# Optimization experiments

Hardware: AMD Instinct MI355X
Metric: run time of the kernel (lower is better)

The kernel has to match this reference:

```python
import jax, jax.numpy as jnp
import numpy as np

B, T, H = 16, 512, 512

def _gru_layer(x, h0, wih, whh, bih, bhh, reverse):
    # x: [B,T,in], h0: [B,H]; PyTorch gate order r,z,n in the 3H axis.
    xg = jnp.einsum('bti,gi->btg', x, wih) + bih  # [B,T,3H] input-side gates, precomputed
    def step(h, xg_t):
        gh = h @ whh.T + bhh  # [B,3H]
        xr, xz, xn = jnp.split(xg_t, 3, axis=-1)
        hr, hz, hn = jnp.split(gh, 3, axis=-1)
        r = jax.nn.sigmoid(xr + hr)
        z = jax.nn.sigmoid(xz + hz)
        n = jnp.tanh(xn + r * hn)
        h_new = (1.0 - z) * n + z * h
        return h_new, h_new
    _, ys = jax.lax.scan(step, h0, jnp.swapaxes(xg, 0, 1), reverse=reverse)  # [T,B,H]
    return jnp.swapaxes(ys, 0, 1)

def _forward(x, h1, h2,
             wih_l0f, whh_l0f, bih_l0f, bhh_l0f, wih_l0b, whh_l0b, bih_l0b, bhh_l0b,
             wih_l1f, whh_l1f, bih_l1f, bhh_l1f, wih_l1b, whh_l1b, bih_l1b, bhh_l1b,
             wih_l2f, whh_l2f, bih_l2f, bhh_l2f, wih_l2b, whh_l2b, bih_l2b, bhh_l2b,
             g2_wih, g2_whh, g2_bih, g2_bhh, fc_w, fc_b):
    layers = [((wih_l0f, whh_l0f, bih_l0f, bhh_l0f), (wih_l0b, whh_l0b, bih_l0b, bhh_l0b)),
              ((wih_l1f, whh_l1f, bih_l1f, bhh_l1f), (wih_l1b, whh_l1b, bih_l1b, bhh_l1b)),
              ((wih_l2f, whh_l2f, bih_l2f, bhh_l2f), (wih_l2b, whh_l2b, bih_l2b, bhh_l2b))]
    out = x
    for l, (pf, pb) in enumerate(layers):
        of = _gru_layer(out, h1[2 * l], *pf, reverse=False)
        ob = _gru_layer(out, h1[2 * l + 1], *pb, reverse=True)
        out = jnp.concatenate([of, ob], axis=-1)  # [B,T,2H]
    out2 = _gru_layer(out, h2[0], g2_wih, g2_whh, g2_bih, g2_bhh, reverse=False)  # [B,T,H]
    logits = out2[:, -1, :] @ fc_w.T + fc_b  # [B,1]
    return (jax.nn.sigmoid(logits), out2)

def setup_inputs():
    key = jax.random.key(0)
    ks = jax.random.split(key, 40)
    cnt = iter(range(40))
    s = jnp.float32(0.04)
    d = {}
    d['x'] = jax.random.normal(ks[next(cnt)], (B, T, 2048), jnp.float32)
    d['h1'] = jax.random.normal(ks[next(cnt)], (6, B, H), jnp.float32) * s
    d['h2'] = jax.random.normal(ks[next(cnt)], (1, B, H), jnp.float32) * s
    in_dims = [2048, 2 * H, 2 * H]
    for l in range(3):
        for dr in 'fb':
            d[f'wih_l{l}{dr}'] = jax.random.normal(ks[next(cnt)], (3 * H, in_dims[l]), jnp.float32) * s
            d[f'whh_l{l}{dr}'] = jax.random.normal(ks[next(cnt)], (3 * H, H), jnp.float32) * s
            d[f'bih_l{l}{dr}'] = jax.random.normal(ks[next(cnt)], (3 * H,), jnp.float32) * s
            d[f'bhh_l{l}{dr}'] = jax.random.normal(ks[next(cnt)], (3 * H,), jnp.float32) * s
    d['g2_wih'] = jax.random.normal(ks[next(cnt)], (3 * H, 2 * H), jnp.float32) * s
    d['g2_whh'] = jax.random.normal(ks[next(cnt)], (3 * H, H), jnp.float32) * s
    d['g2_bih'] = jax.random.normal(ks[next(cnt)], (3 * H,), jnp.float32) * s
    d['g2_bhh'] = jax.random.normal(ks[next(cnt)], (3 * H,), jnp.float32) * s
    d['fc_w'] = jax.random.normal(ks[next(cnt)], (1, H), jnp.float32) * s
    d['fc_b'] = jax.random.normal(ks[next(cnt)], (1,), jnp.float32) * s
    return d

def reference(x, h1, h2,
              wih_l0f, whh_l0f, bih_l0f, bhh_l0f, wih_l0b, whh_l0b, bih_l0b, bhh_l0b,
              wih_l1f, whh_l1f, bih_l1f, bhh_l1f, wih_l1b, whh_l1b, bih_l1b, bhh_l1b,
              wih_l2f, whh_l2f, bih_l2f, bhh_l2f, wih_l2b, whh_l2b, bih_l2b, bhh_l2b,
              g2_wih, g2_whh, g2_bih, g2_bhh, fc_w, fc_b):
    return _forward(x, h1, h2,
                    wih_l0f, whh_l0f, bih_l0f, bhh_l0f, wih_l0b, whh_l0b, bih_l0b, bhh_l0b,
                    wih_l1f, whh_l1f, bih_l1f, bhh_l1f, wih_l1b, whh_l1b, bih_l1b, bhh_l1b,
                    wih_l2f, whh_l2f, bih_l2f, bhh_l2f, wih_l2b, whh_l2b, bih_l2b, bhh_l2b,
                    g2_wih, g2_whh, g2_bih, g2_bhh, fc_w, fc_b)
```

## Files before the change

### kernel.cpp

```cpp
#include <hip/hip_runtime.h>
#include <cstdint>
#include <cstddef>

typedef unsigned short u16;
typedef unsigned int u32;
typedef __attribute__((ext_vector_type(8))) short bf16x8;
typedef __attribute__((ext_vector_type(4))) float f32x4;

#define T_SEQ 512
#define HID 512

__device__ __forceinline__ u16 f2bf(float f) {
  union { float f; u32 i; } c; c.f = f;
  u32 r = (c.i + 0x7FFFu + ((c.i >> 16) & 1u)) >> 16;
  return (u16)r;
}
__device__ __forceinline__ u16 f2h(float f) {
  union { _Float16 h; u16 u; } c; c.h = (_Float16)f; return c.u;
}
__device__ __forceinline__ float h2f(u16 u) {
  union { u16 u; _Float16 h; } c; c.u = u; return (float)c.h;
}
__device__ __forceinline__ float sigmf(float x) { return 1.f / (1.f + __expf(-x)); }
__device__ __forceinline__ float tanhfast(float x) {
  float e = __expf(2.f * x); return 1.f - 2.f / (e + 1.f);
}

template <int AF32>
__launch_bounds__(256)
__global__ void gemm_xg(const void* __restrict__ Av,
                        const float* __restrict__ W0, const float* __restrict__ W1,
                        const float* __restrict__ b0, const float* __restrict__ b1,
                        u16* __restrict__ xg0, u16* __restrict__ xg1, int K) {
  const int dir = blockIdx.z;
  const float* W = dir ? W1 : W0;
  const float* bias = dir ? b1 : b0;
  u16* xg = dir ? xg1 : xg0;
  const int bm = blockIdx.x, bn = blockIdx.y;
  const int tid = threadIdx.x, lane = tid & 63, wv = tid >> 6;
  const int wm = wv & 1, wn = wv >> 1, quad = lane >> 4, l15 = lane & 15;

  __shared__ u16 As[128 * 40];
  __shared__ u16 Bs[128 * 40];

  f32x4 acc[4][4] = {};
  const float* Wb = W + (size_t)(bn * 128) * K;

  for (int k0 = 0; k0 < K; k0 += 32) {
    __syncthreads();
    if constexpr (AF32) {
      const float* Ab = (const float*)Av + (size_t)(bm * 128) * K;
#pragma unroll
      for (int it = 0; it < 4; ++it) {
        int c = tid + it * 256;
        int row = c >> 3, kp = (c & 7) * 4;
        float4 v = *(const float4*)(Ab + (size_t)row * K + k0 + kp);
        ushort4 s = { f2bf(v.x), f2bf(v.y), f2bf(v.z), f2bf(v.w) };
        *(ushort4*)(&As[row * 40 + kp]) = s;
      }
    } else {
      const u16* Ab = (const u16*)Av + (size_t)(bm * 128) * K;
#pragma unroll
      for (int it = 0; it < 2; ++it) {
        int c = tid + it * 256;
        int row = c >> 2, kp = (c & 3) * 8;
        *(bf16x8*)(&As[row * 40 + kp]) = *(const bf16x8*)(Ab + (size_t)row * K + k0 + kp);
      }
    }
#pragma unroll
    for (int it = 0; it < 4; ++it) {
      int c = tid + it * 256;
      int row = c >> 3, kp = (c & 7) * 4;
      float4 v = *(const float4*)(Wb + (size_t)row * K + k0 + kp);
      ushort4 s = { f2bf(v.x), f2bf(v.y), f2bf(v.z), f2bf(v.w) };
      *(ushort4*)(&Bs[row * 40 + kp]) = s;
    }
    __syncthreads();
    bf16x8 af[4], bf[4];
#pragma unroll
    for (int i = 0; i < 4; ++i) {
      af[i] = *(const bf16x8*)(&As[(wm * 64 + i * 16 + l15) * 40 + quad * 8]);
      bf[i] = *(const bf16x8*)(&Bs[(wn * 64 + i * 16 + l15) * 40 + quad * 8]);
    }
#pragma unroll
    for (int mi = 0; mi < 4; ++mi)
#pragma unroll
      for (int ni = 0; ni < 4; ++ni)
        acc[mi][ni] = __builtin_amdgcn_mfma_f32_16x16x32_bf16(af[mi], bf[ni], acc[mi][ni], 0, 0, 0);
  }

#pragma unroll
  for (int ni = 0; ni < 4; ++ni) {
    int n = bn * 128 + wn * 64 + ni * 16 + l15;
    float bv = bias[n];
#pragma unroll
    for (int mi = 0; mi < 4; ++mi) {
      int m0 = bm * 128 + wm * 64 + mi * 16 + quad * 4;
#pragma unroll
      for (int r = 0; r < 4; ++r)
        xg[(size_t)(m0 + r) * 1536 + n] = f2h(acc[mi][ni][r] + bv);
    }
  }
}

__launch_bounds__(384, 1)
__global__ void gru_rec(const u16* __restrict__ xg_f, const u16* __restrict__ xg_b,
                        const float* __restrict__ whh_f, const float* __restrict__ whh_b,
                        const float* __restrict__ bhh_f, const float* __restrict__ bhh_b,
                        const float* __restrict__ h0_f, const float* __restrict__ h0_b,
                        void* __restrict__ outp, int out_stride, int out_f32,
                        u16* __restrict__ hbuf, int* __restrict__ counters, int Tn) {
  const int dir = blockIdx.y;
  const u16* xg   = dir ? xg_b  : xg_f;
  const float* whh = dir ? whh_b : whh_f;
  const float* bhh = dir ? bhh_b : bhh_f;
  const float* h0  = dir ? h0_b  : h0_f;
  const int w = blockIdx.x;
  const int tid = threadIdx.x, lane = tid & 63, wv = tid >> 6;
  const int quad = lane >> 4, l15 = lane & 15;
  int* cnt = counters + dir * 1024;
  u16* hb0 = hbuf + (dir * 2 + 0) * (16 * 512);
  u16* hb1 = hbuf + (dir * 2 + 1) * (16 * 512);
  const int dir_off = dir * 512;

  __shared__ float glds[3][16][64];
  __shared__ float hprev[16][64];
  __shared__ u16 xlds[3][16][64];
  __shared__ float bhl[3][64];

  bf16x8 bfr[2][16];
#pragma unroll
  for (int f = 0; f < 2; ++f) {
    int fl = wv * 2 + f;
    int g = fl >> 2, q = fl & 3;
    int row = g * 512 + (w * 4 + q) * 16 + l15;
    const float* wp = whh + (size_t)row * 512 + quad * 8;
#pragma unroll
    for (int kt = 0; kt < 16; ++kt) {
      float4 a = *(const float4*)(wp + kt * 32);
      float4 b = *(const float4*)(wp + kt * 32 + 4);
      bf16x8 fr;
      fr[0] = (short)f2bf(a.x); fr[1] = (short)f2bf(a.y);
      fr[2] = (short)f2bf(a.z); fr[3] = (short)f2bf(a.w);
      fr[4] = (short)f2bf(b.x); fr[5] = (short)f2bf(b.y);
      fr[6] = (short)f2bf(b.z); fr[7] = (short)f2bf(b.w);
      bfr[f][kt] = fr;
    }
  }
  for (int i = tid; i < 512; i += 384) {
    int b = i >> 5, j2 = (i & 31) * 2;
    float v0 = h0[b * 512 + w * 64 + j2];
    float v1 = h0[b * 512 + w * 64 + j2 + 1];
    hprev[b][j2] = v0; hprev[b][j2 + 1] = v1;
    u32 pk = (u32)f2bf(v0) | ((u32)f2bf(v1) << 16);
    __hip_atomic_store((u32*)(hb1 + b * 512 + w * 64 + j2), pk,
                       __ATOMIC_RELAXED, __HIP_MEMORY_SCOPE_AGENT);
  }
  for (int i = tid; i < 192; i += 384) {
    int g = i >> 6, jl = i & 63;
    bhl[g][jl] = bhh[g * 512 + w * 64 + jl];
  }
  __syncthreads();
  if (tid == 0)
    __hip_atomic_fetch_add(&cnt[0], 1, __ATOMIC_RELEASE, __HIP_MEMORY_SCOPE_AGENT);

  for (int t = 0; t < Tn; ++t) {
    const int te = dir ? (Tn - 1 - t) : t;
    for (int i = tid; i < 768; i += 384) {
      int g = i >> 8, r2 = i & 255, b = r2 >> 4, j4 = (r2 & 15) * 4;
      uint2 v = *(const uint2*)(xg + ((size_t)(b * Tn + te)) * 1536 + g * 512 + w * 64 + j4);
      *(uint2*)(&xlds[g][b][j4]) = v;
    }
    if (tid == 0) {
      while (__hip_atomic_load(&cnt[t], __ATOMIC_RELAXED, __HIP_MEMORY_SCOPE_AGENT) < 8)
        __builtin_amdgcn_s_sleep(1);
      (void)__hip_atomic_load(&cnt[t], __ATOMIC_ACQUIRE, __HIP_MEMORY_SCOPE_AGENT);
    }
    __syncthreads();

    const u16* hsrc = (t & 1) ? hb0 : hb1;
    const u16* hp = hsrc + l15 * 512 + quad * 8;
    bf16x8 afr[16];
#pragma unroll
    for (int kt = 0; kt < 16; ++kt) afr[kt] = *(const bf16x8*)(hp + kt * 32);

#pragma unroll
    for (int f = 0; f < 2; ++f) {
      f32x4 acc = {0.f, 0.f, 0.f, 0.f};
#pragma unroll
      for (int kt = 0; kt < 16; ++kt)
        acc = __builtin_amdgcn_mfma_f32_16x16x32_bf16(afr[kt], bfr[f][kt], acc, 0, 0, 0);
      int fl = wv * 2 + f, g = fl >> 2, q = fl & 3;
#pragma unroll
      for (int r = 0; r < 4; ++r) glds[g][quad * 4 + r][q * 16 + l15] = acc[r];
    }
    __syncthreads();

    u16* hbw = (t & 1) ? hb1 : hb0;
    for (int i = tid; i < 512; i += 384) {
      int b = i >> 5, j2 = (i & 31) * 2;
      float hn2[2];
#pragma unroll
      for (int u = 0; u < 2; ++u) {
        int jl = j2 + u;
        float xr = h2f(xlds[0][b][jl]);
        float xz = h2f(xlds[1][b][jl]);
        float xn = h2f(xlds[2][b][jl]);
        float hr = glds[0][b][jl] + bhl[0][jl];
        float hz = glds[1][b][jl] + bhl[1][jl];
        float hnn = glds[2][b][jl] + bhl[2][jl];
        float r = sigmf(xr + hr);
        float z = sigmf(xz + hz);
        float n = tanhfast(xn + r * hnn);
        float hv = (1.f - z) * n + z * hprev[b][jl];
        hprev[b][jl] = hv;
        hn2[u] = hv;
      }
      u32 pk = (u32)f2bf(hn2[0]) | ((u32)f2bf(hn2[1]) << 16);
      __hip_atomic_store((u32*)(hbw + b * 512 + w * 64 + j2), pk,
                         __ATOMIC_RELAXED, __HIP_MEMORY_SCOPE_AGENT);
      if (out_f32) {
        float2 o = { hn2[0], hn2[1] };
        *(float2*)((float*)outp + (size_t)(b * Tn + te) * out_stride + dir_off + w * 64 + j2) = o;
      } else {
        *(u32*)((u16*)outp + (size_t)(b * Tn + te) * out_stride + dir_off + w * 64 + j2) = pk;
      }
    }
    __syncthreads();
    if (tid == 0)
      __hip_atomic_fetch_add(&cnt[t + 1], 1, __ATOMIC_RELEASE, __HIP_MEMORY_SCOPE_AGENT);
  }
}

__global__ void fc_kernel(const float* __restrict__ out2, const float* __restrict__ fc_w,
                          const float* __restrict__ fc_b, float* __restrict__ dst) {
  int b = blockIdx.x, lane = threadIdx.x;
  const float* row = out2 + ((size_t)b * T_SEQ + (T_SEQ - 1)) * HID;
  float s = 0.f;
  for (int j = lane; j < HID; j += 64) s += row[j] * fc_w[j];
#pragma unroll
  for (int off = 32; off > 0; off >>= 1) s += __shfl_down(s, off, 64);
  if (lane == 0) dst[b] = sigmf(s + fc_b[0]);
}

extern "C" void kernel_launch(void* const* d_in, const int* in_sizes, int n_in,
                              void* d_out, int out_size, void* d_ws, size_t ws_size,
                              hipStream_t stream) {
  const float* x  = (const float*)d_in[0];
  const float* h1 = (const float*)d_in[1];
  const float* h2 = (const float*)d_in[2];
  auto P = [&](int i) { return (const float*)d_in[i]; };

  u16* xg0 = (u16*)d_ws;
  u16* xg1 = xg0 + (size_t)8192 * 1536;
  u16* outb = xg1 + (size_t)8192 * 1536;
  u16* hbuf = outb + (size_t)8192 * 1024;
  int* counters = (int*)(hbuf + 4 * 8192);
  float* out_f = (float*)d_out;
  float* out2 = out_f + 16;

  hipMemsetAsync(counters, 0, 8192 * sizeof(int), stream);

  gemm_xg<1><<<dim3(64, 12, 2), 256, 0, stream>>>(x, P(3), P(7), P(5), P(9), xg0, xg1, 2048);
  gru_rec<<<dim3(8, 2), 384, 0, stream>>>(xg0, xg1, P(4), P(8), P(6), P(10),
                                          h1, h1 + 8192, outb, 1024, 0, hbuf, counters, T_SEQ);
  gemm_xg<0><<<dim3(64, 12, 2), 256, 0, stream>>>(outb, P(11), P(15), P(13), P(17), xg0, xg1, 1024);
  gru_rec<<<dim3(8, 2), 384, 0, stream>>>(xg0, xg1, P(12), P(16), P(14), P(18),
                                          h1 + 2 * 8192, h1 + 3 * 8192, outb, 1024, 0, hbuf,
                                          counters + 2048, T_SEQ);
  gemm_xg<0><<<dim3(64, 12, 2), 256, 0, stream>>>(outb, P(19), P(23), P(21), P(25), xg0, xg1, 1024);
  gru_rec<<<dim3(8, 2), 384, 0, stream>>>(xg0, xg1, P(20), P(24), P(22), P(26),
                                          h1 + 4 * 8192, h1 + 5 * 8192, outb, 1024, 0, hbuf,
                                          counters + 4096, T_SEQ);
  gemm_xg<0><<<dim3(64, 12, 1), 256, 0, stream>>>(outb, P(27), P(27), P(29), P(29), xg0, xg1, 1024);
  gru_rec<<<dim3(8, 1), 384, 0, stream>>>(xg0, xg0, P(28), P(28), P(30), P(30),
                                          h2, h2, out2, 512, 1, hbuf, counters + 6144, T_SEQ);
  fc_kernel<<<16, 64, 0, stream>>>(out2, P(31), P(32), out_f);
}
```

Before: 11.89 ms.

## Restructure GRU recurrence so each wave owns all three gates with per-wave flags

Rewrites the recurrent kernel so that each wave computes the r, z and n gate columns for its own 16 hidden units. r and z weights stay in registers and the n weights sit in LDS, so the gate nonlinearity runs directly on the MFMA accumulators with no LDS round trip and no block-wide barriers. The grid drops to 4 blocks of 512 threads per direction. Cross-block synchronisation moves from one shared counter per timestep to a flag per wave, polled by a single wave-wide load. The change also prefetches xg straight into registers, and in exchange adds 32-way flag polling and uses 128KB of LDS per block.

```diff
diff --git a/kernel.cpp b/kernel.cpp
--- a/kernel.cpp
+++ b/kernel.cpp
@@ -24,6 +24,16 @@
 __device__ __forceinline__ float sigmf(float x) { return 1.f / (1.f + __expf(-x)); }
 __device__ __forceinline__ float tanhfast(float x) {
   float e = __expf(2.f * x); return 1.f - 2.f / (e + 1.f);
+}
+__device__ __forceinline__ bf16x8 pack8(const float* p) {
+  float4 a = *(const float4*)(p);
+  float4 b = *(const float4*)(p + 4);
+  bf16x8 fr;
+  fr[0] = (short)f2bf(a.x); fr[1] = (short)f2bf(a.y);
+  fr[2] = (short)f2bf(a.z); fr[3] = (short)f2bf(a.w);
+  fr[4] = (short)f2bf(b.x); fr[5] = (short)f2bf(b.y);
+  fr[6] = (short)f2bf(b.z); fr[7] = (short)f2bf(b.w);
+  return fr;
 }
 
 template <int AF32>
@@ -76,17 +86,17 @@
       *(ushort4*)(&Bs[row * 40 + kp]) = s;
     }
     __syncthreads();
-    bf16x8 af[4], bf[4];
+    bf16x8 af[4], bfv[4];
 #pragma unroll
     for (int i = 0; i < 4; ++i) {
       af[i] = *(const bf16x8*)(&As[(wm * 64 + i * 16 + l15) * 40 + quad * 8]);
-      bf[i] = *(const bf16x8*)(&Bs[(wn * 64 + i * 16 + l15) * 40 + quad * 8]);
+      bfv[i] = *(const bf16x8*)(&Bs[(wn * 64 + i * 16 + l15) * 40 + quad * 8]);
     }
 #pragma unroll
     for (int mi = 0; mi < 4; ++mi)
 #pragma unroll
       for (int ni = 0; ni < 4; ++ni)
-        acc[mi][ni] = __builtin_amdgcn_mfma_f32_16x16x32_bf16(af[mi], bf[ni], acc[mi][ni], 0, 0, 0);
+        acc[mi][ni] = __builtin_amdgcn_mfma_f32_16x16x32_bf16(af[mi], bfv[ni], acc[mi][ni], 0, 0, 0);
   }
 
 #pragma unroll
@@ -103,7 +113,7 @@
   }
 }
 
-__launch_bounds__(384, 1)
+__launch_bounds__(512, 2)
 __global__ void gru_rec(const u16* __restrict__ xg_f, const u16* __restrict__ xg_b,
                         const float* __restrict__ whh_f, const float* __restrict__ whh_b,
                         const float* __restrict__ bhh_f, const float* __restrict__ bhh_b,
@@ -118,117 +128,123 @@
   const int w = blockIdx.x;
   const int tid = threadIdx.x, lane = tid & 63, wv = tid >> 6;
   const int quad = lane >> 4, l15 = lane & 15;
-  int* cnt = counters + dir * 1024;
+  const int gcol = w * 128 + wv * 16 + l15;
+  int* flg = counters + dir * 1024;
   u16* hb0 = hbuf + (dir * 2 + 0) * (16 * 512);
   u16* hb1 = hbuf + (dir * 2 + 1) * (16 * 512);
   const int dir_off = dir * 512;
 
-  __shared__ float glds[3][16][64];
-  __shared__ float hprev[16][64];
-  __shared__ u16 xlds[3][16][64];
-  __shared__ float bhl[3][64];
+  __shared__ u16 nlds[8 * 8192];
 
   bf16x8 bfr[2][16];
-#pragma unroll
-  for (int f = 0; f < 2; ++f) {
-    int fl = wv * 2 + f;
-    int g = fl >> 2, q = fl & 3;
-    int row = g * 512 + (w * 4 + q) * 16 + l15;
-    const float* wp = whh + (size_t)row * 512 + quad * 8;
+  {
+    const float* wr = whh + (size_t)(0 * 512 + gcol) * 512 + quad * 8;
+    const float* wz = whh + (size_t)(1 * 512 + gcol) * 512 + quad * 8;
+    const float* wn = whh + (size_t)(2 * 512 + gcol) * 512 + quad * 8;
 #pragma unroll
     for (int kt = 0; kt < 16; ++kt) {
-      float4 a = *(const float4*)(wp + kt * 32);
-      float4 b = *(const float4*)(wp + kt * 32 + 4);
-      bf16x8 fr;
-      fr[0] = (short)f2bf(a.x); fr[1] = (short)f2bf(a.y);
-      fr[2] = (short)f2bf(a.z); fr[3] = (short)f2bf(a.w);
-      fr[4] = (short)f2bf(b.x); fr[5] = (short)f2bf(b.y);
-      fr[6] = (short)f2bf(b.z); fr[7] = (short)f2bf(b.w);
-      bfr[f][kt] = fr;
-    }
-  }
-  for (int i = tid; i < 512; i += 384) {
-    int b = i >> 5, j2 = (i & 31) * 2;
-    float v0 = h0[b * 512 + w * 64 + j2];
-    float v1 = h0[b * 512 + w * 64 + j2 + 1];
-    hprev[b][j2] = v0; hprev[b][j2 + 1] = v1;
-    u32 pk = (u32)f2bf(v0) | ((u32)f2bf(v1) << 16);
-    __hip_atomic_store((u32*)(hb1 + b * 512 + w * 64 + j2), pk,
-                       __ATOMIC_RELAXED, __HIP_MEMORY_SCOPE_AGENT);
-  }
-  for (int i = tid; i < 192; i += 384) {
-    int g = i >> 6, jl = i & 63;
-    bhl[g][jl] = bhh[g * 512 + w * 64 + jl];
-  }
-  __syncthreads();
-  if (tid == 0)
-    __hip_atomic_fetch_add(&cnt[0], 1, __ATOMIC_RELEASE, __HIP_MEMORY_SCOPE_AGENT);
+      bfr[0][kt] = pack8(wr + kt * 32);
+      bfr[1][kt] = pack8(wz + kt * 32);
+      *(bf16x8*)(&nlds[wv * 8192 + kt * 512 + lane * 8]) = pack8(wn + kt * 32);
+    }
+  }
+  const float bh0 = bhh[0 * 512 + gcol];
+  const float bh1 = bhh[1 * 512 + gcol];
+  const float bh2 = bhh[2 * 512 + gcol];
+
+  float hv[4];
+#pragma unroll
+  for (int r = 0; r < 4; ++r) hv[r] = h0[(quad * 4 + r) * 512 + gcol];
+#pragma unroll
+  for (int r = 0; r < 4; ++r) {
+    u32 hb = (u32)f2bf(hv[r]);
+    u32 pb = (u32)__shfl_xor((int)hb, 1, 64);
+    if (!(lane & 1))
+      __hip_atomic_store((u32*)(hb1 + (quad * 4 + r) * 512 + gcol), hb | (pb << 16),
+                         __ATOMIC_RELAXED, __HIP_MEMORY_SCOPE_AGENT);
+  }
+  if (lane == 0)
+    __hip_atomic_store(&flg[w * 8 + wv], 1, __ATOMIC_RELEASE, __HIP_MEMORY_SCOPE_AGENT);
 
   for (int t = 0; t < Tn; ++t) {
     const int te = dir ? (Tn - 1 - t) : t;
-    for (int i = tid; i < 768; i += 384) {
-      int g = i >> 8, r2 = i & 255, b = r2 >> 4, j4 = (r2 & 15) * 4;
-      uint2 v = *(const uint2*)(xg + ((size_t)(b * Tn + te)) * 1536 + g * 512 + w * 64 + j4);
-      *(uint2*)(&xlds[g][b][j4]) = v;
-    }
-    if (tid == 0) {
-      while (__hip_atomic_load(&cnt[t], __ATOMIC_RELAXED, __HIP_MEMORY_SCOPE_AGENT) < 8)
+
+    u16 xv[12];
+    {
+      const u16* xb = xg + (size_t)te * 1536 + gcol;
+#pragma unroll
+      for (int r = 0; r < 4; ++r)
+#pragma unroll
+        for (int g = 0; g < 3; ++g)
+          xv[r * 3 + g] = xb[(size_t)(quad * 4 + r) * Tn * 1536 + g * 512];
+    }
+
+    {
+      const int target = t + 1;
+      while (1) {
+        int v = (lane < 32)
+            ? __hip_atomic_load(&flg[lane], __ATOMIC_RELAXED, __HIP_MEMORY_SCOPE_AGENT)
+            : 0x7fffffff;
+        if (__all(v >= target)) break;
         __builtin_amdgcn_s_sleep(1);
-      (void)__hip_atomic_load(&cnt[t], __ATOMIC_ACQUIRE, __HIP_MEMORY_SCOPE_AGENT);
-    }
-    __syncthreads();
-
-    const u16* hsrc = (t & 1) ? hb0 : hb1;
-    const u16* hp = hsrc + l15 * 512 + quad * 8;
+      }
+      __builtin_amdgcn_fence(__ATOMIC_ACQUIRE, "agent");
+    }
+
+    const u16* hp = ((t & 1) ? hb0 : hb1) + l15 * 512 + quad * 8;
     bf16x8 afr[16];
 #pragma unroll
     for (int kt = 0; kt < 16; ++kt) afr[kt] = *(const bf16x8*)(hp + kt * 32);
 
-#pragma unroll
-    for (int f = 0; f < 2; ++f) {
-      f32x4 acc = {0.f, 0.f, 0.f, 0.f};
-#pragma unroll
-      for (int kt = 0; kt < 16; ++kt)
-        acc = __builtin_amdgcn_mfma_f32_16x16x32_bf16(afr[kt], bfr[f][kt], acc, 0, 0, 0);
-      int fl = wv * 2 + f, g = fl >> 2, q = fl & 3;
-#pragma unroll
-      for (int r = 0; r < 4; ++r) glds[g][quad * 4 + r][q * 16 + l15] = acc[r];
-    }
-    __syncthreads();
+    f32x4 accr = {0.f, 0.f, 0.f, 0.f}, accz = accr, accn = accr;
+#pragma unroll
+    for (int kt = 0; kt < 16; ++kt) {
+      bf16x8 nf = *(const bf16x8*)(&nlds[wv * 8192 + kt * 512 + lane * 8]);
+      accr = __builtin_amdgcn_mfma_f32_16x16x32_bf16(afr[kt], bfr[0][kt], accr, 0, 0, 0);
+      accz = __builtin_amdgcn_mfma_f32_16x16x32_bf16(afr[kt], bfr[1][kt], accz, 0, 0, 0);
+      accn = __builtin_amdgcn_mfma_f32_16x16x32_bf16(afr[kt], nf, accn, 0, 0, 0);
+    }
+
+#pragma unroll
+    for (int r = 0; r < 4; ++r) {
+      float xr = h2f(xv[r * 3 + 0]);
+      float xz = h2f(xv[r * 3 + 1]);
+      float xn = h2f(xv[r * 3 + 2]);
+      float rg = sigmf(xr + accr[r] + bh0);
+      float zg = sigmf(xz + accz[r] + bh1);
+      float ng = tanhfast(xn + rg * (accn[r] + bh2));
+      hv[r] = (1.f - zg) * ng + zg * hv[r];
+    }
 
     u16* hbw = (t & 1) ? hb1 : hb0;
-    for (int i = tid; i < 512; i += 384) {
-      int b = i >> 5, j2 = (i & 31) * 2;
-      float hn2[2];
-#pragma unroll
-      for (int u = 0; u < 2; ++u) {
-        int jl = j2 + u;
-        float xr = h2f(xlds[0][b][jl]);
-        float xz = h2f(xlds[1][b][jl]);
-        float xn = h2f(xlds[2][b][jl]);
-        float hr = glds[0][b][jl] + bhl[0][jl];
-        float hz = glds[1][b][jl] + bhl[1][jl];
-        float hnn = glds[2][b][jl] + bhl[2][jl];
-        float r = sigmf(xr + hr);
-        float z = sigmf(xz + hz);
-        float n = tanhfast(xn + r * hnn);
-        float hv = (1.f - z) * n + z * hprev[b][jl];
-        hprev[b][jl] = hv;
-        hn2[u] = hv;
-      }
-      u32 pk = (u32)f2bf(hn2[0]) | ((u32)f2bf(hn2[1]) << 16);
-      __hip_atomic_store((u32*)(hbw + b * 512 + w * 64 + j2), pk,
-                         __ATOMIC_RELAXED, __HIP_MEMORY_SCOPE_AGENT);
-      if (out_f32) {
-        float2 o = { hn2[0], hn2[1] };
-        *(float2*)((float*)outp + (size_t)(b * Tn + te) * out_stride + dir_off + w * 64 + j2) = o;
-      } else {
-        *(u32*)((u16*)outp + (size_t)(b * Tn + te) * out_stride + dir_off + w * 64 + j2) = pk;
-      }
-    }
-    __syncthreads();
-    if (tid == 0)
-      __hip_atomic_fetch_add(&cnt[t + 1], 1, __ATOMIC_RELEASE, __HIP_MEMORY_SCOPE_AGENT);
+    u32 opk[4];
+#pragma unroll
+    for (int r = 0; r < 4; ++r) {
+      u32 hb = (u32)f2bf(hv[r]);
+      u32 pb = (u32)__shfl_xor((int)hb, 1, 64);
+      opk[r] = hb | (pb << 16);
+      if (!(lane & 1))
+        __hip_atomic_store((u32*)(hbw + (quad * 4 + r) * 512 + gcol), opk[r],
+                           __ATOMIC_RELAXED, __HIP_MEMORY_SCOPE_AGENT);
+    }
+    if (lane == 0)
+      __hip_atomic_store(&flg[w * 8 + wv], t + 2, __ATOMIC_RELEASE, __HIP_MEMORY_SCOPE_AGENT);
+
+    if (out_f32) {
+#pragma unroll
+      for (int r = 0; r < 4; ++r) {
+        float pf = __shfl_xor(hv[r], 1, 64);
+        if (!(lane & 1)) {
+          float2 o = { hv[r], pf };
+          *(float2*)((float*)outp + (size_t)((quad * 4 + r) * Tn + te) * out_stride + dir_off + gcol) = o;
+        }
+      }
+    } else {
+#pragma unroll
+      for (int r = 0; r < 4; ++r)
+        if (!(lane & 1))
+          *(u32*)((u16*)outp + (size_t)((quad * 4 + r) * Tn + te) * out_stride + dir_off + gcol) = opk[r];
+    }
   }
 }
 
@@ -262,18 +278,18 @@
   hipMemsetAsync(counters, 0, 8192 * sizeof(int), stream);
 
   gemm_xg<1><<<dim3(64, 12, 2), 256, 0, stream>>>(x, P(3), P(7), P(5), P(9), xg0, xg1, 2048);
-  gru_rec<<<dim3(8, 2), 384, 0, stream>>>(xg0, xg1, P(4), P(8), P(6), P(10),
+  gru_rec<<<dim3(4, 2), 512, 0, stream>>>(xg0, xg1, P(4), P(8), P(6), P(10),
                                           h1, h1 + 8192, outb, 1024, 0, hbuf, counters, T_SEQ);
   gemm_xg<0><<<dim3(64, 12, 2), 256, 0, stream>>>(outb, P(11), P(15), P(13), P(17), xg0, xg1, 1024);
-  gru_rec<<<dim3(8, 2), 384, 0, stream>>>(xg0, xg1, P(12), P(16), P(14), P(18),
+  gru_rec<<<dim3(4, 2), 512, 0, stream>>>(xg0, xg1, P(12), P(16), P(14), P(18),
                                           h1 + 2 * 8192, h1 + 3 * 8192, outb, 1024, 0, hbuf,
                                           counters + 2048, T_SEQ);
   gemm_xg<0><<<dim3(64, 12, 2), 256, 0, stream>>>(outb, P(19), P(23), P(21), P(25), xg0, xg1, 1024);
-  gru_rec<<<dim3(8, 2), 384, 0, stream>>>(xg0, xg1, P(20), P(24), P(22), P(26),
+  gru_rec<<<dim3(4, 2), 512, 0, stream>>>(xg0, xg1, P(20), P(24), P(22), P(26),
                                           h1 + 4 * 8192, h1 + 5 * 8192, outb, 1024, 0, hbuf,
                                           counters + 4096, T_SEQ);
   gemm_xg<0><<<dim3(64, 12, 1), 256, 0, stream>>>(outb, P(27), P(27), P(29), P(29), xg0, xg1, 1024);
-  gru_rec<<<dim3(8, 1), 384, 0, stream>>>(xg0, xg0, P(28), P(28), P(30), P(30),
+  gru_rec<<<dim3(4, 1), 512, 0, stream>>>(xg0, xg0, P(28), P(28), P(30), P(30),
                                           h2, h2, out2, 512, 1, hbuf, counters + 6144, T_SEQ);
   fc_kernel<<<16, 64, 0, stream>>>(out2, P(31), P(32), out_f);
 }
```

After: 18.31 ms. 1.54x slower.
